# Optimization experiments

Hardware: AMD Instinct MI355X
Metric: run time of the kernel (lower is better)

The kernel has to match this reference:

```python
import jax, jax.numpy as jnp
import numpy as np

B, L, DIM, HEADS, DIM_HEAD = 16, 1024, 512, 8, 64


def _make_perms(rng):
    # perm = identity on first DIM indices, random permutation of [DIM, L*DIM) after
    perms = []
    for _ in range(HEADS - 1):
        tail = rng.permutation(np.arange(DIM, L * DIM))
        perms.append(np.concatenate([np.arange(DIM), tail]))
    return jnp.asarray(np.stack(perms), dtype=jnp.int64)


def setup_inputs() -> dict:
    key = jax.random.key(0)
    ks = jax.random.split(key, 6)
    s = 0.02
    return {
        "x": jax.random.normal(ks[0], (B, L, DIM), dtype=jnp.float32),
        "perms": _make_perms(np.random.default_rng(0)),
        "Wq": jax.random.normal(ks[1], (HEADS, DIM, DIM_HEAD), dtype=jnp.float32) * s,
        "Wk": jax.random.normal(ks[2], (HEADS, DIM, DIM_HEAD), dtype=jnp.float32) * s,
        "Wv": jax.random.normal(ks[3], (HEADS, DIM, DIM_HEAD), dtype=jnp.float32) * s,
        "Wo": jax.random.normal(ks[4], (DIM, HEADS * DIM_HEAD), dtype=jnp.float32) * s,
        "bo": jnp.zeros((DIM,), dtype=jnp.float32),
    }


def reference(x, perms, Wq, Wk, Wv, Wo, bo):
    b, l, d = x.shape
    h, _, e = Wq.shape
    scale = e ** -0.5
    # shuffled query inputs for heads 1..h-1
    flat = x.reshape(b, l * d)                      # [B, L*D]
    shuf = flat[:, perms].reshape(b, h - 1, l, d)   # [B, H-1, L, D]
    xq = jnp.concatenate([x[:, None], shuf], axis=1)  # [B, H, L, D]
    q = jnp.einsum('bhld,hde->bhle', xq, Wq)
    k = jnp.einsum('bld,hde->bhle', x, Wk)
    v = jnp.einsum('bld,hde->bhle', x, Wv)
    attn = jax.nn.softmax(jnp.einsum('bhqe,bhke->bhqk', q, k) * scale, axis=-1)
    out = jnp.einsum('bhqk,bhke->bhqe', attn, v)    # [B, H, L, E]
    out = out.transpose(0, 2, 1, 3).reshape(b, l, h * e)  # concat heads on last dim
    return jnp.einsum('bli,di->bld', out, Wo) + bo
```

## Files before the change

kernel.cpp:

```cpp
#include <hip/hip_runtime.h>

#define LL 1024
#define DD 512
#define HH 8
#define EE 64
#define LDX (LL*DD)
#define BB 16

typedef _Float16 h8 __attribute__((ext_vector_type(8)));
typedef _Float16 h4 __attribute__((ext_vector_type(4)));
typedef float f4 __attribute__((ext_vector_type(4)));
typedef int i4 __attribute__((ext_vector_type(4)));

__device__ __forceinline__ f4 mfma16(h8 a, h8 b, f4 c) {
    return __builtin_amdgcn_mfma_f32_16x16x32_f16(a, b, c, 0, 0, 0);
}

__global__ __launch_bounds__(256) void k_prep(
    const float* __restrict__ x, _Float16* __restrict__ xT)
{
    const int s = blockIdx.x * 256 + threadIdx.x;
    h8 lo, hi;
    #pragma unroll
    for (int b = 0; b < 8; ++b)  lo[b] = (_Float16)x[(size_t)b*LDX + s];
    #pragma unroll
    for (int b = 0; b < 8; ++b)  hi[b] = (_Float16)x[(size_t)(b+8)*LDX + s];
    _Float16* d = xT + (size_t)s * BB;
    *(h8*)d = lo; *(h8*)(d + 8) = hi;
}

__global__ __launch_bounds__(256) void k_x16(
    const float* __restrict__ x, _Float16* __restrict__ x16)
{
    const int i = blockIdx.x * 256 + threadIdx.x;
    f4 v = ((const f4*)x)[i];
    h4 o;
    #pragma unroll
    for (int j = 0; j < 4; ++j) o[j] = (_Float16)v[j];
    *(h4*)(x16 + 4*(size_t)i) = o;
}

__global__ __launch_bounds__(256) void k_wprep(
    const float* __restrict__ Wq, const float* __restrict__ Wk,
    const float* __restrict__ Wv, _Float16* __restrict__ WT)
{
    const int d0 = blockIdx.x * 64;
    const int zz = blockIdx.y;
    const float* src; float sc = 1.f;
    if (zz < 8)       src = Wk + (size_t)zz*DD*EE;
    else if (zz < 16) src = Wv + (size_t)(zz-8)*DD*EE;
    else            { src = Wq + (size_t)(zz-16)*DD*EE; sc = 0.18033688011112042f; }
    const int t = threadIdx.x;
    const int e = t & 63, dq = t >> 6;
    #pragma unroll
    for (int i = 0; i < 16; ++i) {
        int d = d0 + dq*16 + i;
        WT[(size_t)(zz*64 + e)*DD + d] = (_Float16)(src[(size_t)d*EE + e] * sc);
    }
}

__global__ __launch_bounds__(256) void k_wo16(
    const float* __restrict__ Wo, _Float16* __restrict__ Wo16)
{
    const int i = blockIdx.x * 256 + threadIdx.x;
    f4 v = ((const f4*)Wo)[i];
    #pragma unroll
    for (int j = 0; j < 4; ++j) Wo16[4*i + j] = (_Float16)v[j];
}

__global__ __launch_bounds__(256) void k_qkv(
    const _Float16* __restrict__ x16, const _Float16* __restrict__ WT,
    _Float16* __restrict__ qw, _Float16* __restrict__ kw, _Float16* __restrict__ vw)
{
    const int y  = blockIdx.x;
    const int r0 = blockIdx.y * 128;

    __shared__ __align__(16) _Float16 As[2][128][72];
    __shared__ __align__(16) _Float16 Bs[2][128][72];

    const int t = threadIdx.x;
    const int wv = t >> 6, lane = t & 63;
    const int m = lane & 15, qd = lane >> 4;
    const int sr = t >> 1, sc0 = (t & 1) * 32;

    const _Float16* ax = x16 + (size_t)(r0 + sr)*DD + sc0;
    const _Float16* bx = WT  + (size_t)(y*128 + sr)*DD + sc0;

    #pragma unroll
    for (int c = 0; c < 4; ++c) {
        *(h8*)&As[0][sr][sc0 + 8*c] = *(const h8*)(ax + 8*c);
        *(h8*)&Bs[0][sr][sc0 + 8*c] = *(const h8*)(bx + 8*c);
    }
    __syncthreads();

    f4 acc[2][8] = {};
    int cur = 0;
    for (int kt = 0; kt < 8; ++kt) {
        const int alt = cur ^ 1;
        h8 an[4], bn[4];
        if (kt < 7) {
            const _Float16* a2 = ax + (kt+1)*64;
            const _Float16* b2 = bx + (kt+1)*64;
            #pragma unroll
            for (int c = 0; c < 4; ++c) {
                an[c] = *(const h8*)(a2 + 8*c);
                bn[c] = *(const h8*)(b2 + 8*c);
            }
        }
        #pragma unroll
        for (int ks = 0; ks < 2; ++ks) {
            h8 a0 = *(const h8*)&As[cur][32*wv +  0 + m][32*ks + 8*qd];
            h8 a1 = *(const h8*)&As[cur][32*wv + 16 + m][32*ks + 8*qd];
            #pragma unroll
            for (int nt = 0; nt < 8; ++nt) {
                h8 bb = *(const h8*)&Bs[cur][16*nt + m][32*ks + 8*qd];
                acc[0][nt] = mfma16(a0, bb, acc[0][nt]);
                acc[1][nt] = mfma16(a1, bb, acc[1][nt]);
            }
        }
        if (kt < 7) {
            #pragma unroll
            for (int c = 0; c < 4; ++c) {
                *(h8*)&As[alt][sr][sc0 + 8*c] = an[c];
                *(h8*)&Bs[alt][sr][sc0 + 8*c] = bn[c];
            }
            __syncthreads();
            cur = alt;
        }
    }

    #pragma unroll
    for (int nt = 0; nt < 8; ++nt) {
        const int n = y*128 + 16*nt + m;
        const int z = n >> 6, e = n & 63;
        if (z >= 17) continue;
        _Float16* dst; int h;
        if (z < 8)       { dst = kw; h = z; }
        else if (z < 16) { dst = vw; h = z - 8; }
        else             { dst = qw; h = 0; }
        dst += (size_t)h*LL*EE + e;
        #pragma unroll
        for (int mt = 0; mt < 2; ++mt)
            #pragma unroll
            for (int r = 0; r < 4; ++r) {
                int R = r0 + 32*wv + 16*mt + 4*qd + r;
                int b = R >> 10, l = R & 1023;
                dst[((size_t)b*HH*LL + l)*EE] = (_Float16)acc[mt][nt][r];
            }
    }
}

__global__ __launch_bounds__(256) void k_qshuf(
    const _Float16* __restrict__ xT, const int* __restrict__ perms,
    const _Float16* __restrict__ WT, _Float16* __restrict__ qw)
{
    const int l0 = blockIdx.x * 4;
    const int h  = blockIdx.y + 1;
    const _Float16* Wb = WT + (size_t)((16 + h)*64)*DD;
    const int* pbase = perms + (size_t)(h-1)*LDX;

    __shared__ __align__(16) _Float16 As[2][64][72];
    __shared__ __align__(16) _Float16 Bs[2][64][72];

    const int t = threadIdx.x;
    const int wv = t >> 6, lane = t & 63;
    const int m = lane & 15, qd = lane >> 4;
    const int lg = t >> 6, kcol = t & 63;
    const int br = t >> 2, bc0 = (t & 3) * 16;

    int pv[8];
    #pragma unroll
    for (int kt = 0; kt < 8; ++kt)
        pv[kt] = pbase[(size_t)(l0 + lg)*DD + kt*64 + kcol];

    h8 g0p[3], g1p[3], b0p[3], b1p[3];
    #pragma unroll
    for (int j = 0; j < 3; ++j) {
        const _Float16* g = xT + (size_t)pv[j] * BB;
        g0p[j] = *(const h8*)g; g1p[j] = *(const h8*)(g + 8);
        const _Float16* s = Wb + (size_t)br*DD + j*64 + bc0;
        b0p[j] = *(const h8*)s; b1p[j] = *(const h8*)(s + 8);
    }

    *(h8*)&Bs[0][br][bc0]     = b0p[0];
    *(h8*)&Bs[0][br][bc0 + 8] = b1p[0];
    #pragma unroll
    for (int i = 0; i < 8; ++i) As[0][lg*16 + i][kcol]     = g0p[0][i];
    #pragma unroll
    for (int i = 0; i < 8; ++i) As[0][lg*16 + 8 + i][kcol] = g1p[0][i];
    __syncthreads();

    f4 acc[4] = {};
    #pragma unroll
    for (int kt = 0; kt < 8; ++kt) {
        const int cur = kt & 1;
        if (kt + 3 < 8) {
            const int st = (kt + 3) % 3;
            const _Float16* g = xT + (size_t)pv[kt+3] * BB;
            g0p[st] = *(const h8*)g; g1p[st] = *(const h8*)(g + 8);
            const _Float16* s = Wb + (size_t)br*DD + (kt+3)*64 + bc0;
            b0p[st] = *(const h8*)s; b1p[st] = *(const h8*)(s + 8);
        }
        #pragma unroll
        for (int ks = 0; ks < 2; ++ks) {
            h8 a = *(const h8*)&As[cur][16*wv + m][32*ks + 8*qd];
            #pragma unroll
            for (int nt = 0; nt < 4; ++nt) {
                h8 bb = *(const h8*)&Bs[cur][16*nt + m][32*ks + 8*qd];
                acc[nt] = mfma16(a, bb, acc[nt]);
            }
        }
        if (kt < 7) {
            const int alt = cur ^ 1;
            const int st = (kt + 1) % 3;
            *(h8*)&Bs[alt][br][bc0]     = b0p[st];
            *(h8*)&Bs[alt][br][bc0 + 8] = b1p[st];
            #pragma unroll
            for (int i = 0; i < 8; ++i) As[alt][lg*16 + i][kcol]     = g0p[st][i];
            #pragma unroll
            for (int i = 0; i < 8; ++i) As[alt][lg*16 + 8 + i][kcol] = g1p[st][i];
            __syncthreads();
        }
    }

    #pragma unroll
    for (int nt = 0; nt < 4; ++nt)
        #pragma unroll
        for (int r = 0; r < 4; ++r) {
            int b = 4*qd + r;
            qw[((size_t)(b*HH + h)*LL + l0 + wv)*EE + 16*nt + m] = (_Float16)acc[nt][r];
        }
}

__global__ __launch_bounds__(256, 4) void k_attn(
    const _Float16* __restrict__ qw, const _Float16* __restrict__ kw,
    const _Float16* __restrict__ vw, _Float16* __restrict__ oa)
{
    const int bh = blockIdx.x;
    const int l0 = blockIdx.y * 128;
    const int b = bh >> 3, h = bh & 7;
    const _Float16* qb = qw + ((size_t)bh*LL + l0)*EE;
    const _Float16* kb = kw + (size_t)bh*LL*EE;
    const _Float16* vb = vw + (size_t)bh*LL*EE;

    __shared__ __align__(16) _Float16 KsF[2][64*64];
    __shared__ __align__(16) _Float16 VtsF[2][64*64];

    const int t = threadIdx.x;
    const int wv = t >> 6, lane = t & 63;
    const int m = lane & 15, qd = lane >> 4;
    const int m7 = m & 7;
    const int qdp = ((qd & 1) << 1) | (qd >> 1);
    const int krow = t >> 2, c0 = t & 3;
    const int vkey = t & 63, vec = t >> 6;
    const int vhi = vkey >> 3, vlo = vkey & 7;

    h8 qa[2][2];
    #pragma unroll
    for (int mt = 0; mt < 2; ++mt)
        #pragma unroll
        for (int ks = 0; ks < 2; ++ks)
            qa[mt][ks] = *(const h8*)(qb + (size_t)(32*wv + 16*mt + m)*EE + 32*ks + 8*qd);

    f4 oacc[2][4] = {};
    f4 lpacc[2] = {};
    h8 ones;
    #pragma unroll
    for (int i = 0; i < 8; ++i) ones[i] = (_Float16)1.f;

    {
        const _Float16* sk = kb + (size_t)krow*EE + 16*c0;
        h8 k0 = *(const h8*)sk, k1 = *(const h8*)(sk + 8);
        const _Float16* sv = vb + (size_t)vkey*EE + 16*vec;
        h8 v0 = *(const h8*)sv, v1 = *(const h8*)(sv + 8);
        *(h8*)&KsF[0][(krow<<6) + 8*((2*c0)     ^ (krow & 7))] = k0;
        *(h8*)&KsF[0][(krow<<6) + 8*((2*c0 + 1) ^ (krow & 7))] = k1;
        #pragma unroll
        for (int i = 0; i < 8; ++i)
            VtsF[0][((16*vec + i)<<6)     + 8*(vhi ^ i) + vlo] = v0[i];
        #pragma unroll
        for (int i = 0; i < 8; ++i)
            VtsF[0][((16*vec + 8 + i)<<6) + 8*(vhi ^ i) + vlo] = v1[i];
    }
    __syncthreads();

    for (int kt = 0; kt < 16; ++kt) {
        const int cur = kt & 1, alt = cur ^ 1;
        h8 kn0, kn1, vn0, vn1;
        if (kt < 15) {
            const _Float16* sk = kb + (size_t)((kt+1)*64 + krow)*EE + 16*c0;
            kn0 = *(const h8*)sk; kn1 = *(const h8*)(sk + 8);
            const _Float16* sv = vb + (size_t)((kt+1)*64 + vkey)*EE + 16*vec;
            vn0 = *(const h8*)sv; vn1 = *(const h8*)(sv + 8);
        }

        f4 sacc[2][4] = {};
        #pragma unroll
        for (int ks = 0; ks < 2; ++ks)
            #pragma unroll
            for (int nt = 0; nt < 4; ++nt) {
                h8 kf = *(const h8*)&KsF[cur][((16*nt + m)<<6) + 8*((4*ks + qd) ^ m7)];
                sacc[0][nt] = mfma16(kf, qa[0][ks], sacc[0][nt]);
                sacc[1][nt] = mfma16(kf, qa[1][ks], sacc[1][nt]);
            }

        unsigned E[2][4][2];
        #pragma unroll
        for (int mt = 0; mt < 2; ++mt)
            #pragma unroll
            for (int nt = 0; nt < 4; ++nt) {
                float e0 = __builtin_amdgcn_exp2f(sacc[mt][nt][0]);
                float e1 = __builtin_amdgcn_exp2f(sacc[mt][nt][1]);
                float e2 = __builtin_amdgcn_exp2f(sacc[mt][nt][2]);
                float e3 = __builtin_amdgcn_exp2f(sacc[mt][nt][3]);
                E[mt][nt][0] = __builtin_bit_cast(unsigned, __builtin_amdgcn_cvt_pkrtz(e0, e1));
                E[mt][nt][1] = __builtin_bit_cast(unsigned, __builtin_amdgcn_cvt_pkrtz(e2, e3));
            }

        h8 pa[2][2];
        #pragma unroll
        for (int mt = 0; mt < 2; ++mt)
            #pragma unroll
            for (int ks = 0; ks < 2; ++ks) {
                auto x = __builtin_amdgcn_permlane16_swap(E[mt][2*ks][0], E[mt][2*ks+1][0], false, false);
                auto y = __builtin_amdgcn_permlane16_swap(E[mt][2*ks][1], E[mt][2*ks+1][1], false, false);
                i4 pw;
                pw[0] = (int)x[0]; pw[1] = (int)y[0]; pw[2] = (int)x[1]; pw[3] = (int)y[1];
                pa[mt][ks] = __builtin_bit_cast(h8, pw);
            }

        #pragma unroll
        for (int ks = 0; ks < 2; ++ks) {
            #pragma unroll
            for (int nt = 0; nt < 4; ++nt) {
                h8 vf = *(const h8*)&VtsF[cur][((16*nt + m)<<6) + 8*((4*ks + qdp) ^ m7)];
                oacc[0][nt] = mfma16(pa[0][ks], vf, oacc[0][nt]);
                oacc[1][nt] = mfma16(pa[1][ks], vf, oacc[1][nt]);
            }
            lpacc[0] = mfma16(pa[0][ks], ones, lpacc[0]);
            lpacc[1] = mfma16(pa[1][ks], ones, lpacc[1]);
        }

        if (kt < 15) {
            *(h8*)&KsF[alt][(krow<<6) + 8*((2*c0)     ^ (krow & 7))] = kn0;
            *(h8*)&KsF[alt][(krow<<6) + 8*((2*c0 + 1) ^ (krow & 7))] = kn1;
            #pragma unroll
            for (int i = 0; i < 8; ++i)
                VtsF[alt][((16*vec + i)<<6)     + 8*(vhi ^ i) + vlo] = vn0[i];
            #pragma unroll
            for (int i = 0; i < 8; ++i)
                VtsF[alt][((16*vec + 8 + i)<<6) + 8*(vhi ^ i) + vlo] = vn1[i];
            __syncthreads();
        }
    }

    _Float16* ob = oa + ((size_t)(b*LL + l0))*(HH*EE) + h*EE;
    #pragma unroll
    for (int mt = 0; mt < 2; ++mt)
        #pragma unroll
        for (int r = 0; r < 4; ++r) {
            const float inv = __builtin_amdgcn_rcpf(lpacc[mt][r]);
            #pragma unroll
            for (int nt = 0; nt < 4; ++nt) {
                int row = 32*wv + 16*mt + 4*qd + r;
                ob[(size_t)row*(HH*EE) + 16*nt + m] = (_Float16)(oacc[mt][nt][r] * inv);
            }
        }
}

__global__ __launch_bounds__(256) void k_oproj(
    const _Float16* __restrict__ oa, const _Float16* __restrict__ Wo16,
    const float* __restrict__ bo, float* __restrict__ out)
{
    const int y  = blockIdx.x;
    const int r0 = blockIdx.y * 128;

    __shared__ __align__(16) _Float16 As[2][128][72];
    __shared__ __align__(16) _Float16 Bs[2][128][72];

    const int t = threadIdx.x;
    const int wv = t >> 6, lane = t & 63;
    const int m = lane & 15, qd = lane >> 4;
    const int sr = t >> 1, sc0 = (t & 1) * 32;

    const _Float16* ax = oa   + (size_t)(r0 + sr)*DD + sc0;
    const _Float16* bx = Wo16 + (size_t)(y*128 + sr)*DD + sc0;

    #pragma unroll
    for (int c = 0; c < 4; ++c) {
        *(h8*)&As[0][sr][sc0 + 8*c] = *(const h8*)(ax + 8*c);
        *(h8*)&Bs[0][sr][sc0 + 8*c] = *(const h8*)(bx + 8*c);
    }
    __syncthreads();

    f4 acc[2][8] = {};
    int cur = 0;
    for (int kt = 0; kt < 8; ++kt) {
        const int alt = cur ^ 1;
        h8 an[4], bn[4];
        if (kt < 7) {
            const _Float16* a2 = ax + (kt+1)*64;
            const _Float16* b2 = bx + (kt+1)*64;
            #pragma unroll
            for (int c = 0; c < 4; ++c) {
                an[c] = *(const h8*)(a2 + 8*c);
                bn[c] = *(const h8*)(b2 + 8*c);
            }
        }
        #pragma unroll
        for (int ks = 0; ks < 2; ++ks) {
            h8 a0 = *(const h8*)&As[cur][32*wv +  0 + m][32*ks + 8*qd];
            h8 a1 = *(const h8*)&As[cur][32*wv + 16 + m][32*ks + 8*qd];
            #pragma unroll
            for (int nt = 0; nt < 8; ++nt) {
                h8 bb = *(const h8*)&Bs[cur][16*nt + m][32*ks + 8*qd];
                acc[0][nt] = mfma16(a0, bb, acc[0][nt]);
                acc[1][nt] = mfma16(a1, bb, acc[1][nt]);
            }
        }
        if (kt < 7) {
            #pragma unroll
            for (int c = 0; c < 4; ++c) {
                *(h8*)&As[alt][sr][sc0 + 8*c] = an[c];
                *(h8*)&Bs[alt][sr][sc0 + 8*c] = bn[c];
            }
            __syncthreads();
            cur = alt;
        }
    }

    #pragma unroll
    for (int nt = 0; nt < 8; ++nt) {
        const int col = y*128 + 16*nt + m;
        const float bias = bo[col];
        #pragma unroll
        for (int mt = 0; mt < 2; ++mt)
            #pragma unroll
            for (int r = 0; r < 4; ++r) {
                int row = 32*wv + 16*mt + 4*qd + r;
                out[(size_t)(r0 + row)*DD + col] = acc[mt][nt][r] + bias;
            }
    }
}

extern "C" void kernel_launch(void* const* d_in, const int* in_sizes, int n_in,
                              void* d_out, int out_size, void* d_ws, size_t ws_size,
                              hipStream_t stream)
{
    const float* x  = (const float*)d_in[0];
    const int*   pm = (const int*)d_in[1];
    const float* Wq = (const float*)d_in[2];
    const float* Wk = (const float*)d_in[3];
    const float* Wv = (const float*)d_in[4];
    const float* Wo = (const float*)d_in[5];
    const float* bo = (const float*)d_in[6];
    float* out = (float*)d_out;

    const size_t QS = (size_t)BB * HH * LL * EE;
    _Float16* q    = (_Float16*)d_ws;
    _Float16* k    = q + QS;
    _Float16* v    = k + QS;
    _Float16* oaw  = v + QS;
    _Float16* xT   = oaw;
    _Float16* WT   = oaw + QS;
    _Float16* Wo16 = WT + (size_t)24*64*DD;
    _Float16* x16  = (_Float16*)d_out;

    k_x16  <<<dim3(LDX*BB/1024),    256, 0, stream>>>(x, x16);
    k_prep <<<dim3(LDX/256),        256, 0, stream>>>(x, xT);
    k_wprep<<<dim3(8, 24),          256, 0, stream>>>(Wq, Wk, Wv, WT);
    k_wo16 <<<dim3(DD*DD/1024),     256, 0, stream>>>(Wo, Wo16);
    k_qkv  <<<dim3(9, BB*LL/128),   256, 0, stream>>>(x16, WT, q, k, v);
    k_qshuf<<<dim3(LL/4, HH-1),     256, 0, stream>>>(xT, pm, WT, q);
    k_attn <<<dim3(BB*HH, LL/128),  256, 0, stream>>>(q, k, v, oaw);
    k_oproj<<<dim3(DD/128, BB*LL/128), 256, 0, stream>>>(oaw, Wo16, bo, out);
}
```

Baseline: 279.0 us.

## Merge prep kernels and interleave QKV and shuffled-Q GEMMs into one launch

Folds the four conversion/prep kernels into a single launch that dispatches on block index, and combines the QKV projection and shuffled-query projection kernels into one launch whose blocks are interleaved (9 QKV blocks to 14 shuffle blocks per group). The aim is to cut launch overhead and tail idle time, and to let the compute-bound GEMM blocks overlap with the gather-heavy shuffle blocks. The combined kernel reserves the larger shared-memory footprint for every block, which could lower occupancy for the shuffle part.

```diff
diff --git a/kernel.cpp b/kernel.cpp
--- a/kernel.cpp
+++ b/kernel.cpp
@@ -16,67 +16,61 @@
     return __builtin_amdgcn_mfma_f32_16x16x32_f16(a, b, c, 0, 0, 0);
 }
 
-__global__ __launch_bounds__(256) void k_prep(
-    const float* __restrict__ x, _Float16* __restrict__ xT)
-{
-    const int s = blockIdx.x * 256 + threadIdx.x;
-    h8 lo, hi;
-    #pragma unroll
-    for (int b = 0; b < 8; ++b)  lo[b] = (_Float16)x[(size_t)b*LDX + s];
-    #pragma unroll
-    for (int b = 0; b < 8; ++b)  hi[b] = (_Float16)x[(size_t)(b+8)*LDX + s];
-    _Float16* d = xT + (size_t)s * BB;
-    *(h8*)d = lo; *(h8*)(d + 8) = hi;
-}
-
-__global__ __launch_bounds__(256) void k_x16(
-    const float* __restrict__ x, _Float16* __restrict__ x16)
-{
-    const int i = blockIdx.x * 256 + threadIdx.x;
-    f4 v = ((const f4*)x)[i];
-    h4 o;
-    #pragma unroll
-    for (int j = 0; j < 4; ++j) o[j] = (_Float16)v[j];
-    *(h4*)(x16 + 4*(size_t)i) = o;
-}
-
-__global__ __launch_bounds__(256) void k_wprep(
-    const float* __restrict__ Wq, const float* __restrict__ Wk,
-    const float* __restrict__ Wv, _Float16* __restrict__ WT)
-{
-    const int d0 = blockIdx.x * 64;
-    const int zz = blockIdx.y;
-    const float* src; float sc = 1.f;
-    if (zz < 8)       src = Wk + (size_t)zz*DD*EE;
-    else if (zz < 16) src = Wv + (size_t)(zz-8)*DD*EE;
-    else            { src = Wq + (size_t)(zz-16)*DD*EE; sc = 0.18033688011112042f; }
+__global__ __launch_bounds__(256) void k_prep_all(
+    const float* __restrict__ x,  const float* __restrict__ Wq,
+    const float* __restrict__ Wk, const float* __restrict__ Wv,
+    const float* __restrict__ Wo,
+    _Float16* __restrict__ x16, _Float16* __restrict__ xT,
+    _Float16* __restrict__ WT,  _Float16* __restrict__ Wo16)
+{
+    const int bx = blockIdx.x;
     const int t = threadIdx.x;
-    const int e = t & 63, dq = t >> 6;
-    #pragma unroll
-    for (int i = 0; i < 16; ++i) {
-        int d = d0 + dq*16 + i;
-        WT[(size_t)(zz*64 + e)*DD + d] = (_Float16)(src[(size_t)d*EE + e] * sc);
-    }
-}
-
-__global__ __launch_bounds__(256) void k_wo16(
-    const float* __restrict__ Wo, _Float16* __restrict__ Wo16)
-{
-    const int i = blockIdx.x * 256 + threadIdx.x;
-    f4 v = ((const f4*)Wo)[i];
-    #pragma unroll
-    for (int j = 0; j < 4; ++j) Wo16[4*i + j] = (_Float16)v[j];
-}
-
-__global__ __launch_bounds__(256) void k_qkv(
+    if (bx < 8192) {
+        const int i = bx * 256 + t;
+        f4 v = ((const f4*)x)[i];
+        h4 o;
+        #pragma unroll
+        for (int j = 0; j < 4; ++j) o[j] = (_Float16)v[j];
+        *(h4*)(x16 + 4*(size_t)i) = o;
+    } else if (bx < 8192 + 2048) {
+        const int s = (bx - 8192) * 256 + t;
+        h8 lo, hi;
+        #pragma unroll
+        for (int b = 0; b < 8; ++b)  lo[b] = (_Float16)x[(size_t)b*LDX + s];
+        #pragma unroll
+        for (int b = 0; b < 8; ++b)  hi[b] = (_Float16)x[(size_t)(b+8)*LDX + s];
+        _Float16* d = xT + (size_t)s * BB;
+        *(h8*)d = lo; *(h8*)(d + 8) = hi;
+    } else if (bx < 8192 + 2048 + 192) {
+        const int id = bx - (8192 + 2048);
+        const int d0 = (id & 7) * 64;
+        const int zz = id >> 3;
+        const float* src; float sc = 1.f;
+        if (zz < 8)       src = Wk + (size_t)zz*DD*EE;
+        else if (zz < 16) src = Wv + (size_t)(zz-8)*DD*EE;
+        else            { src = Wq + (size_t)(zz-16)*DD*EE; sc = 0.18033688011112042f; }
+        const int e = t & 63, dq = t >> 6;
+        #pragma unroll
+        for (int i = 0; i < 16; ++i) {
+            int d = d0 + dq*16 + i;
+            WT[(size_t)(zz*64 + e)*DD + d] = (_Float16)(src[(size_t)d*EE + e] * sc);
+        }
+    } else {
+        const int i = (bx - (8192 + 2048 + 192)) * 256 + t;
+        f4 v = ((const f4*)Wo)[i];
+        #pragma unroll
+        for (int j = 0; j < 4; ++j) Wo16[4*i + j] = (_Float16)v[j];
+    }
+}
+
+__device__ __forceinline__ void qkv_body(
+    int y, int r0,
     const _Float16* __restrict__ x16, const _Float16* __restrict__ WT,
-    _Float16* __restrict__ qw, _Float16* __restrict__ kw, _Float16* __restrict__ vw)
-{
-    const int y  = blockIdx.x;
-    const int r0 = blockIdx.y * 128;
-
-    __shared__ __align__(16) _Float16 As[2][128][72];
-    __shared__ __align__(16) _Float16 Bs[2][128][72];
+    _Float16* __restrict__ qw, _Float16* __restrict__ kw, _Float16* __restrict__ vw,
+    _Float16* smem)
+{
+    auto As = (_Float16(*)[128][72])smem;
+    auto Bs = (_Float16(*)[128][72])(smem + 2*128*72);
 
     const int t = threadIdx.x;
     const int wv = t >> 6, lane = t & 63;
@@ -150,17 +144,17 @@
     }
 }
 
-__global__ __launch_bounds__(256) void k_qshuf(
+__device__ __forceinline__ void qshuf_body(
+    int l0, int h,
     const _Float16* __restrict__ xT, const int* __restrict__ perms,
-    const _Float16* __restrict__ WT, _Float16* __restrict__ qw)
-{
-    const int l0 = blockIdx.x * 4;
-    const int h  = blockIdx.y + 1;
+    const _Float16* __restrict__ WT, _Float16* __restrict__ qw,
+    _Float16* smem)
+{
+    auto As = (_Float16(*)[64][72])smem;
+    auto Bs = (_Float16(*)[64][72])(smem + 2*64*72);
+
     const _Float16* Wb = WT + (size_t)((16 + h)*64)*DD;
     const int* pbase = perms + (size_t)(h-1)*LDX;
-
-    __shared__ __align__(16) _Float16 As[2][64][72];
-    __shared__ __align__(16) _Float16 Bs[2][64][72];
 
     const int t = threadIdx.x;
     const int wv = t >> 6, lane = t & 63;
@@ -230,6 +224,23 @@
             int b = 4*qd + r;
             qw[((size_t)(b*HH + h)*LL + l0 + wv)*EE + 16*nt + m] = (_Float16)acc[nt][r];
         }
+}
+
+__global__ __launch_bounds__(256) void k_qkv_qshuf(
+    const _Float16* __restrict__ x16, const _Float16* __restrict__ xT,
+    const int* __restrict__ perms, const _Float16* __restrict__ WT,
+    _Float16* __restrict__ qw, _Float16* __restrict__ kw, _Float16* __restrict__ vw)
+{
+    __shared__ __align__(16) _Float16 smem[4*128*72];
+    const int bx = blockIdx.x;
+    const int g = bx / 23, pos = bx % 23;
+    if (pos < 9) {
+        const int qid = g*9 + pos;
+        qkv_body(qid % 9, (qid / 9) * 128, x16, WT, qw, kw, vw, smem);
+    } else {
+        const int sid = g*14 + (pos - 9);
+        qshuf_body((sid & 255) * 4, (sid >> 8) + 1, xT, perms, WT, qw, smem);
+    }
 }
 
 __global__ __launch_bounds__(256, 4) void k_attn(
@@ -466,12 +477,9 @@
     _Float16* Wo16 = WT + (size_t)24*64*DD;
     _Float16* x16  = (_Float16*)d_out;
 
-    k_x16  <<<dim3(LDX*BB/1024),    256, 0, stream>>>(x, x16);
-    k_prep <<<dim3(LDX/256),        256, 0, stream>>>(x, xT);
-    k_wprep<<<dim3(8, 24),          256, 0, stream>>>(Wq, Wk, Wv, WT);
-    k_wo16 <<<dim3(DD*DD/1024),     256, 0, stream>>>(Wo, Wo16);
-    k_qkv  <<<dim3(9, BB*LL/128),   256, 0, stream>>>(x16, WT, q, k, v);
-    k_qshuf<<<dim3(LL/4, HH-1),     256, 0, stream>>>(xT, pm, WT, q);
-    k_attn <<<dim3(BB*HH, LL/128),  256, 0, stream>>>(q, k, v, oaw);
-    k_oproj<<<dim3(DD/128, BB*LL/128), 256, 0, stream>>>(oaw, Wo16, bo, out);
-}
+    k_prep_all <<<dim3(8192 + 2048 + 192 + 256), 256, 0, stream>>>(
+        x, Wq, Wk, Wv, Wo, x16, xT, WT, Wo16);
+    k_qkv_qshuf<<<dim3(2944),            256, 0, stream>>>(x16, xT, pm, WT, q, k, v);
+    k_attn     <<<dim3(BB*HH, LL/128),   256, 0, stream>>>(q, k, v, oaw);
+    k_oproj    <<<dim3(DD/128, BB*LL/128), 256, 0, stream>>>(oaw, Wo16, bo, out);
+}
```

After: 273.1 us. 2.1% less time.
